# Optimization experiments

Measured on AMD Instinct MI355X. Metric: run time of the kernel, lower is better.

## Reference

```python
import jax, jax.numpy as jnp
import numpy as np

N, E, B, T, C_IN, K, F_CHEB, F_T, TS = 2000, 32000, 8, 12, 32, 3, 64, 64, 1
EPS = 1e-5  # torch nn.LayerNorm default


def setup_inputs() -> dict:
    key = jax.random.key(0)
    ks = jax.random.split(key, 12)
    X = jax.random.normal(ks[0], (B, N, C_IN, T), dtype=jnp.float32)
    edge_index = jax.random.randint(ks[1], (2, E), 0, N)
    edge_weight = jax.random.uniform(ks[2], (E,), dtype=jnp.float32)
    # lambda_max of L = D - A (PyG get_laplacian, normalization=None):
    # deg over source rows; power iteration emulates scipy.eigs(which='LM').
    src, dst = edge_index[0], edge_index[1]
    deg = jax.ops.segment_sum(edge_weight, src, num_segments=N)
    rows = jnp.concatenate([src, jnp.arange(N)])
    cols = jnp.concatenate([dst, jnp.arange(N)])
    wL = jnp.concatenate([-edge_weight, deg])
    v = jnp.ones((N,), jnp.float32) / np.sqrt(N)
    lam = jnp.float32(1.0)
    for _ in range(60):
        v2 = jax.ops.segment_sum(wL * v[cols], rows, num_segments=N)
        lam = jnp.linalg.norm(v2)
        v = v2 / (lam + 1e-12)
    lambda_max = lam.reshape(1)
    W_cheb = jax.random.normal(ks[3], (K, C_IN, F_CHEB), dtype=jnp.float32) * 0.1
    b_cheb = jax.random.uniform(ks[4], (F_CHEB,), dtype=jnp.float32) * 0.1
    time_w = jax.random.normal(ks[5], (F_T, F_CHEB, 1, 3), dtype=jnp.float32) * 0.05
    time_b = jax.random.uniform(ks[6], (F_T,), dtype=jnp.float32) * 0.1
    res_w = jax.random.normal(ks[7], (F_T, C_IN, 1, 1), dtype=jnp.float32) * 0.1
    res_b = jax.random.uniform(ks[8], (F_T,), dtype=jnp.float32) * 0.1
    ln_g = jnp.ones((F_T,), jnp.float32)
    ln_b = jnp.zeros((F_T,), jnp.float32)
    return dict(X=X, edge_index=edge_index, edge_weight=edge_weight,
                lambda_max=lambda_max, W_cheb=W_cheb, b_cheb=b_cheb,
                time_w=time_w, time_b=time_b, res_w=res_w, res_b=res_b,
                ln_g=ln_g, ln_b=ln_b)


def reference(X, edge_index, edge_weight, lambda_max, W_cheb, b_cheb,
              time_w, time_b, res_w, res_b, ln_g, ln_b):
    Bd, Nd, Cd, Td = X.shape
    src, dst = edge_index[0], edge_index[1]
    # L = D - A  (deg over source rows, matching PyG get_laplacian)
    deg = jax.ops.segment_sum(edge_weight, src, num_segments=Nd)
    srcs = jnp.concatenate([src, jnp.arange(Nd)])
    dsts = jnp.concatenate([dst, jnp.arange(Nd)])
    w = jnp.concatenate([-edge_weight, deg])
    w = 2.0 * w / lambda_max[0]
    w = w - (srcs == dsts).astype(w.dtype)  # L_hat = 2L/lmax - I

    # faithful to torch_geometric_temporal's permute+reshape of X into [T*B, N, C]
    Xt = jnp.transpose(X, (2, 0, 1, 3)).reshape(Nd, Cd, Td * Bd)
    x0 = Xt.transpose(0, 2, 1)  # node-major [N, T*B, C]

    def prop(h):  # out[dst] += w_e * h[src]  (PyG source_to_target flow)
        return jax.ops.segment_sum(w[:, None, None] * h[srcs], dsts, num_segments=Nd)

    # Chebyshev recursion: T0=x, T1=Lx, Tk=2L T(k-1) - T(k-2)
    out = jnp.einsum('nbc,cf->nbf', x0, W_cheb[0])
    Tx_prev = x0
    Tx = prop(x0)
    out = out + jnp.einsum('nbc,cf->nbf', Tx, W_cheb[1])
    for k in range(2, W_cheb.shape[0]):
        Tx_new = 2.0 * prop(Tx) - Tx_prev
        out = out + jnp.einsum('nbc,cf->nbf', Tx_new, W_cheb[k])
        Tx_prev, Tx = Tx, Tx_new
    out = jax.nn.relu(out + b_cheb)  # [N, T*B, F_cheb]

    # back to [B, N, F_cheb, T]
    Xc = out.transpose(0, 2, 1).reshape(Nd, -1, Bd, Td).transpose(2, 0, 1, 3)
    # temporal conv (1x3, pad (0,1), stride (1,TS)) on [B, F_cheb, N, T]
    h = jax.lax.conv_general_dilated(
        Xc.transpose(0, 2, 1, 3), time_w, (1, TS), ((0, 0), (1, 1)),
        dimension_numbers=('NCHW', 'OIHW', 'NCHW')) + time_b[None, :, None, None]
    # residual 1x1 conv on raw input
    r = jax.lax.conv_general_dilated(
        X.transpose(0, 2, 1, 3), res_w, (1, TS), ((0, 0), (0, 0)),
        dimension_numbers=('NCHW', 'OIHW', 'NCHW')) + res_b[None, :, None, None]
    z = jax.nn.relu(r + h).transpose(0, 3, 2, 1)  # [B, T, N, F_t]
    mu = z.mean(-1, keepdims=True)
    var = ((z - mu) ** 2).mean(-1, keepdims=True)
    z = (z - mu) / jnp.sqrt(var + EPS) * ln_g + ln_b
    return z.transpose(0, 2, 3, 1)  # [B, N, F_t, T]
```

## Files before the change

### kernel.cpp

```cpp
#include <hip/hip_runtime.h>
#include <hip/hip_bf16.h>

#define NN 2000
#define EE 32000
#define TT 12
#define CIN 32
#define FCH 64
#define TB 96
#define NODE_F 3072
#define NODE_F4 768

#define OFF_X0    0
#define OFF_TX1   6144000
#define OFF_CHEB  12288000
#define OFF_DEG   24576000
#define OFF_SW    24578000
#define OFF_ROWP  24580000
#define OFF_CNT   24582048
#define OFF_FILL  24584048
#define OFF_CCOL  24586048
#define OFF_CW    24618048
#define OFF_TWT   24650048
#define OFF_RWT   24662336

__device__ __forceinline__ float comp4(const float4& v, int i) {
  return i == 0 ? v.x : (i == 1 ? v.y : (i == 2 ? v.z : v.w));
}

__device__ __forceinline__ float b2f(unsigned short u) {
  return __uint_as_float(((unsigned)u) << 16);
}

__device__ __forceinline__ unsigned short f2b(float x) {
  __hip_bfloat16 h = __float2bfloat16(x);
  return *(unsigned short*)&h;
}

__global__ __launch_bounds__(256) void k_prep(const float* __restrict__ tw,
    const float* __restrict__ rw, unsigned short* __restrict__ twt,
    unsigned short* __restrict__ rwt) {
  int i = blockIdx.x * 256 + threadIdx.x;
  if (i < 12288) {
    int ft = i / 192;
    int r = i - ft * 192;
    twt[r * 64 + ft] = f2b(tw[i]);
  }
  if (i < 2048) {
    int ft = i >> 5;
    int c = i & 31;
    rwt[c * 64 + ft] = f2b(rw[i]);
  }
}

__global__ __launch_bounds__(256) void k_deg_cnt(const int* __restrict__ src,
    const int* __restrict__ dst, const float* __restrict__ ew,
    float* __restrict__ deg, int* __restrict__ cnt) {
  int e = blockIdx.x * 256 + threadIdx.x;
  if (e < EE) {
    atomicAdd(&deg[src[e]], ew[e]);
    atomicAdd(&cnt[dst[e]], 1);
  }
}

__global__ __launch_bounds__(256) void k_scan(const float* __restrict__ deg,
    const float* __restrict__ lam, const int* __restrict__ cnt,
    float* __restrict__ sw, int* __restrict__ rowp) {
  int tid = threadIdx.x;
  float s = 2.0f / lam[0];
  for (int n = tid; n < NN; n += 256) sw[n] = deg[n] * s - 1.0f;
  __shared__ int part[256];
  int base = tid * 8;
  int local[8];
  int sum = 0;
  #pragma unroll
  for (int i = 0; i < 8; ++i) {
    int idx = base + i;
    int v = (idx < NN) ? cnt[idx] : 0;
    local[i] = sum;
    sum += v;
  }
  part[tid] = sum;
  __syncthreads();
  for (int off = 1; off < 256; off <<= 1) {
    int v = part[tid];
    int add = (tid >= off) ? part[tid - off] : 0;
    __syncthreads();
    part[tid] = v + add;
    __syncthreads();
  }
  int excl = part[tid] - sum;
  #pragma unroll
  for (int i = 0; i < 8; ++i) {
    int idx = base + i;
    if (idx < NN) rowp[idx] = excl + local[i];
  }
  if (tid == 255) rowp[NN] = part[255];
}

__global__ __launch_bounds__(256) void k_fill(const int* __restrict__ src,
    const int* __restrict__ dst, const float* __restrict__ ew,
    const float* __restrict__ lam, const int* __restrict__ rowp,
    int* __restrict__ fill, int* __restrict__ ccol, float* __restrict__ cw) {
  int e = blockIdx.x * 256 + threadIdx.x;
  if (e < EE) {
    float s = 2.0f / lam[0];
    int d = dst[e], sn = src[e];
    int pos = rowp[d] + atomicAdd(&fill[d], 1);
    ccol[pos] = sn;
    cw[pos] = -ew[e] * s - ((sn == d) ? 1.0f : 0.0f);
  }
}

__global__ __launch_bounds__(256) void k_build_x0(const float* __restrict__ X,
                                                  float* __restrict__ x0) {
  int o = blockIdx.x * 256 + threadIdx.x;
  if (o >= NN * NODE_F) return;
  int n = o / NODE_F;
  int rem = o - n * NODE_F;
  int q = rem >> 5;
  int c2 = rem & 31;
  int g = n * NODE_F + c2 * TB + q;
  int ci = g / 192000;
  int r1 = g - ci * 192000;
  int b = r1 / 24000;
  int r2 = r1 - b * 24000;
  int nn2 = r2 / 12;
  int t = r2 - nn2 * 12;
  x0[o] = X[((b * NN + nn2) * CIN + ci) * TT + t];
}

__global__ __launch_bounds__(256) void k_prop1(const float* __restrict__ x0,
    const float* __restrict__ sw, const int* __restrict__ rowp,
    const int* __restrict__ ccol, const float* __restrict__ cw,
    float* __restrict__ tx1) {
  int n = blockIdx.x, tid = threadIdx.x;
  float s = sw[n];
  const float4* xb = (const float4*)x0;
  int own = n * NODE_F4 + tid * 3;
  float4 v0 = xb[own], v1 = xb[own + 1], v2 = xb[own + 2];
  float a[12];
  a[0]=s*v0.x; a[1]=s*v0.y; a[2]=s*v0.z; a[3]=s*v0.w;
  a[4]=s*v1.x; a[5]=s*v1.y; a[6]=s*v1.z; a[7]=s*v1.w;
  a[8]=s*v2.x; a[9]=s*v2.y; a[10]=s*v2.z; a[11]=s*v2.w;
  int rs = rowp[n], re = rowp[n + 1];
  for (int e = rs; e < re; ++e) {
    int c = ccol[e];
    float w = cw[e];
    int cb = c * NODE_F4 + tid * 3;
    float4 u0 = xb[cb], u1 = xb[cb + 1], u2 = xb[cb + 2];
    a[0]+=w*u0.x; a[1]+=w*u0.y; a[2]+=w*u0.z; a[3]+=w*u0.w;
    a[4]+=w*u1.x; a[5]+=w*u1.y; a[6]+=w*u1.z; a[7]+=w*u1.w;
    a[8]+=w*u2.x; a[9]+=w*u2.y; a[10]+=w*u2.z; a[11]+=w*u2.w;
  }
  float4* ob = (float4*)tx1;
  float4 o0, o1, o2;
  o0.x=a[0]; o0.y=a[1]; o0.z=a[2]; o0.w=a[3];
  o1.x=a[4]; o1.y=a[5]; o1.z=a[6]; o1.w=a[7];
  o2.x=a[8]; o2.y=a[9]; o2.z=a[10]; o2.w=a[11];
  ob[own] = o0; ob[own + 1] = o1; ob[own + 2] = o2;
}

__global__ __launch_bounds__(256) void k_cheb(const float* __restrict__ x0,
    const float* __restrict__ tx1, const float* __restrict__ sw,
    const int* __restrict__ rowp, const int* __restrict__ ccol,
    const float* __restrict__ cw, const float* __restrict__ Wc,
    const float* __restrict__ bc, float* __restrict__ cheb) {
  __shared__ float x0l[NODE_F];
  __shared__ float t1l[NODE_F];
  __shared__ float t2l[NODE_F];
  __shared__ __align__(16) unsigned short wl[3 * 2048];
  __shared__ float bl[64];
  int n = blockIdx.x, tid = threadIdx.x;
  {
    const float4* xs = (const float4*)(x0 + (size_t)n * NODE_F);
    const float4* ts = (const float4*)(tx1 + (size_t)n * NODE_F);
    float4* xd = (float4*)x0l;
    float4* td = (float4*)t1l;
    for (int i = tid; i < NODE_F4; i += 256) { xd[i] = xs[i]; td[i] = ts[i]; }
    for (int i = tid; i < 6144; i += 256) wl[i] = f2b(Wc[i]);
    if (tid < 64) bl[tid] = bc[tid];
  }
  float s = sw[n];
  float a[12];
  {
    const float4* tg4 = (const float4*)tx1 + (size_t)n * NODE_F4 + tid * 3;
    float4 v0 = tg4[0], v1 = tg4[1], v2 = tg4[2];
    a[0]=s*v0.x; a[1]=s*v0.y; a[2]=s*v0.z; a[3]=s*v0.w;
    a[4]=s*v1.x; a[5]=s*v1.y; a[6]=s*v1.z; a[7]=s*v1.w;
    a[8]=s*v2.x; a[9]=s*v2.y; a[10]=s*v2.z; a[11]=s*v2.w;
  }
  int rs = rowp[n], re = rowp[n + 1];
  const float4* xb = (const float4*)tx1;
  for (int e = rs; e < re; ++e) {
    int c = ccol[e];
    float w = cw[e];
    int cb = c * NODE_F4 + tid * 3;
    float4 u0 = xb[cb], u1 = xb[cb + 1], u2 = xb[cb + 2];
    a[0]+=w*u0.x; a[1]+=w*u0.y; a[2]+=w*u0.z; a[3]+=w*u0.w;
    a[4]+=w*u1.x; a[5]+=w*u1.y; a[6]+=w*u1.z; a[7]+=w*u1.w;
    a[8]+=w*u2.x; a[9]+=w*u2.y; a[10]+=w*u2.z; a[11]+=w*u2.w;
  }
  __syncthreads();
  #pragma unroll
  for (int j = 0; j < 12; ++j) t2l[tid * 12 + j] = 2.0f * a[j] - x0l[tid * 12 + j];
  __syncthreads();
  int f = tid & 63, qg = tid >> 6;
  float o[24];
  #pragma unroll
  for (int qi = 0; qi < 24; ++qi) o[qi] = bl[f];
  for (int cc = 0; cc < 4; ++cc) {
    float w0r[8], w1r[8], w2r[8];
    #pragma unroll
    for (int i = 0; i < 8; ++i) {
      int c = cc * 8 + i;
      w0r[i] = b2f(wl[c * 64 + f]);
      w1r[i] = b2f(wl[2048 + c * 64 + f]);
      w2r[i] = b2f(wl[4096 + c * 64 + f]);
    }
    #pragma unroll
    for (int qi = 0; qi < 24; ++qi) {
      int q = qi * 4 + qg;
      const float* xr = &x0l[q * 32 + cc * 8];
      const float* t1r = &t1l[q * 32 + cc * 8];
      const float* t2r = &t2l[q * 32 + cc * 8];
      float4 xv0 = *(const float4*)(xr);
      float4 xv1 = *(const float4*)(xr + 4);
      float4 y0 = *(const float4*)(t1r);
      float4 y1 = *(const float4*)(t1r + 4);
      float4 z0 = *(const float4*)(t2r);
      float4 z1 = *(const float4*)(t2r + 4);
      float acc = o[qi];
      #pragma unroll
      for (int i = 0; i < 4; ++i) {
        acc += comp4(xv0, i) * w0r[i] + comp4(y0, i) * w1r[i] + comp4(z0, i) * w2r[i];
        acc += comp4(xv1, i) * w0r[i + 4] + comp4(y1, i) * w1r[i + 4] + comp4(z1, i) * w2r[i + 4];
      }
      o[qi] = acc;
    }
  }
  float* cp = cheb + (size_t)n * TB * FCH;
  #pragma unroll
  for (int qi = 0; qi < 24; ++qi) {
    int q = qi * 4 + qg;
    cp[q * 64 + f] = fmaxf(o[qi], 0.0f);
  }
}

__global__ __launch_bounds__(256, 4) void k_final3(const float* __restrict__ X,
    const float* __restrict__ cheb, const unsigned short* __restrict__ twt,
    const unsigned short* __restrict__ rwt, const float* __restrict__ tb,
    const float* __restrict__ rb, const float* __restrict__ lg,
    const float* __restrict__ lb, float* __restrict__ out) {
  __shared__ float hp[4 * 12 * 64];
  __shared__ float zb[64 * 13];
  int tid = threadIdx.x;
  int f = tid & 63;
  int ntu = __builtin_amdgcn_readfirstlane(tid >> 6);

  float w0[16], w1[16], w2[16];
  #pragma unroll
  for (int i = 0; i < 16; ++i) {
    int fc = ntu * 16 + i;
    w0[i] = b2f(twt[(fc * 3 + 0) * 64 + f]);
    w1[i] = b2f(twt[(fc * 3 + 1) * 64 + f]);
    w2[i] = b2f(twt[(fc * 3 + 2) * 64 + f]);
  }
  float rwv[8];
  #pragma unroll
  for (int i = 0; i < 8; ++i) rwv[i] = b2f(rwt[(ntu * 8 + i) * 64 + f]);
  float tbf = tb[f], rbf = rb[f], lgf = lg[f], lbf = lb[f];
  float hbase = (ntu == 0) ? (tbf + rbf) : 0.0f;

  for (int it = 0; it < 16; ++it) {
    int p = blockIdx.x * 16 + it;
    int b = p / 2000;
    int n = p - b * 2000;
    float h[12];
    #pragma unroll
    for (int t = 0; t < 12; ++t) h[t] = hbase;
    {
      const float4* ch4 = (const float4*)(cheb + (size_t)n * 6144 + b * 768 + ntu * 16);
      #pragma unroll
      for (int r = 0; r < 12; ++r) {
        float4 sa = ch4[r * 16 + 0];
        float4 sb = ch4[r * 16 + 1];
        float4 sc = ch4[r * 16 + 2];
        float4 sd = ch4[r * 16 + 3];
        #pragma unroll
        for (int i = 0; i < 16; ++i) {
          float v = (i < 4) ? comp4(sa, i) : (i < 8) ? comp4(sb, i - 4)
                  : (i < 12) ? comp4(sc, i - 8) : comp4(sd, i - 12);
          if (r <= 10) h[r + 1] += w0[i] * v;
          h[r] += w1[i] * v;
          if (r >= 1) h[r - 1] += w2[i] * v;
        }
      }
    }
    {
      const float4* xp4 = (const float4*)(X + (size_t)p * 384 + ntu * 96);
      #pragma unroll
      for (int ci = 0; ci < 24; ++ci) {
        float4 xv = xp4[ci];
        #pragma unroll
        for (int k = 0; k < 4; ++k) {
          int idx = ci * 4 + k;
          h[idx % 12] += rwv[idx / 12] * comp4(xv, k);
        }
      }
    }
    #pragma unroll
    for (int t = 0; t < 12; ++t) hp[ntu * 768 + t * 64 + f] = h[t];
    __syncthreads();
    #pragma unroll
    for (int tt = 0; tt < 3; ++tt) {
      int t = ntu * 3 + tt;
      float v = hp[t * 64 + f] + hp[768 + t * 64 + f]
              + hp[1536 + t * 64 + f] + hp[2304 + t * 64 + f];
      v = fmaxf(v, 0.0f);
      float sum = v, sq = v * v;
      #pragma unroll
      for (int off = 32; off; off >>= 1) {
        sum += __shfl_xor(sum, off);
        sq += __shfl_xor(sq, off);
      }
      float mu = sum * (1.0f / 64.0f);
      float var = sq * (1.0f / 64.0f) - mu * mu;
      float inv = rsqrtf(var + 1e-5f);
      zb[f * 13 + t] = (v - mu) * inv * lgf + lbf;
    }
    __syncthreads();
    float* op = out + (size_t)p * 768;
    #pragma unroll
    for (int k = 0; k < 3; ++k) {
      int i = tid + k * 256;
      op[i] = zb[(i / 12) * 13 + i % 12];
    }
  }
}

extern "C" void kernel_launch(void* const* d_in, const int* in_sizes, int n_in,
                              void* d_out, int out_size, void* d_ws, size_t ws_size,
                              hipStream_t stream) {
  const float* X   = (const float*)d_in[0];
  const int*   ei  = (const int*)d_in[1];
  const float* ew  = (const float*)d_in[2];
  const float* lam = (const float*)d_in[3];
  const float* Wc  = (const float*)d_in[4];
  const float* bc  = (const float*)d_in[5];
  const float* tw  = (const float*)d_in[6];
  const float* tb  = (const float*)d_in[7];
  const float* rw  = (const float*)d_in[8];
  const float* rb  = (const float*)d_in[9];
  const float* lg  = (const float*)d_in[10];
  const float* lb  = (const float*)d_in[11];
  float* out = (float*)d_out;
  float* ws = (float*)d_ws;
  float* x0   = ws + OFF_X0;
  float* tx1  = ws + OFF_TX1;
  float* cheb = ws + OFF_CHEB;
  float* deg  = ws + OFF_DEG;
  float* swv  = ws + OFF_SW;
  int* rowp = (int*)(ws + OFF_ROWP);
  int* cnt  = (int*)(ws + OFF_CNT);
  int* fill = (int*)(ws + OFF_FILL);
  int* ccol = (int*)(ws + OFF_CCOL);
  float* cwv = ws + OFF_CW;
  unsigned short* twt = (unsigned short*)(ws + OFF_TWT);
  unsigned short* rwt = (unsigned short*)(ws + OFF_RWT);
  const int* srcp = ei;
  const int* dstp = ei + EE;

  hipMemsetAsync(deg, 0, (size_t)(OFF_CCOL - OFF_DEG) * sizeof(float), stream);
  k_prep<<<48, 256, 0, stream>>>(tw, rw, twt, rwt);
  k_deg_cnt<<<(EE + 255) / 256, 256, 0, stream>>>(srcp, dstp, ew, deg, cnt);
  k_scan<<<1, 256, 0, stream>>>(deg, lam, cnt, swv, rowp);
  k_fill<<<(EE + 255) / 256, 256, 0, stream>>>(srcp, dstp, ew, lam, rowp, fill, ccol, cwv);
  k_build_x0<<<(NN * NODE_F + 255) / 256, 256, 0, stream>>>(X, x0);
  k_prop1<<<NN, 256, 0, stream>>>(x0, swv, rowp, ccol, cwv, tx1);
  k_cheb<<<NN, 256, 0, stream>>>(x0, tx1, swv, rowp, ccol, cwv, Wc, bc, cheb);
  k_final3<<<1000, 256, 0, stream>>>(X, cheb, twt, rwt, tb, rb, lg, lb, out);
}
```

Baseline: 407.0 us.

## Store Chebyshev intermediates in bf16 and rebuild x0 transpose through LDS

The x0, Tx1 and Tx2 node feature buffers are now stored as packed bf16 pairs instead of fp32. This halves the bytes moved by the gather-heavy propagation kernels and by the LDS reads in the Chebyshev matmul. k_build_x0 now runs one block per node, loads contiguous float4s and transposes them through shared memory before writing packed bf16, replacing the old scattered per-element gather. k_final3 processes 8 node-batch pairs per block over 2000 blocks instead of 16 over 1000, and the lower precision on intermediates may add numerical error.

```diff
diff --git a/kernel.cpp b/kernel.cpp
--- a/kernel.cpp
+++ b/kernel.cpp
@@ -8,32 +8,35 @@
 #define FCH 64
 #define TB 96
 #define NODE_F 3072
-#define NODE_F4 768
-
-#define OFF_X0    0
-#define OFF_TX1   6144000
-#define OFF_CHEB  12288000
-#define OFF_DEG   24576000
-#define OFF_SW    24578000
-#define OFF_ROWP  24580000
-#define OFF_CNT   24582048
-#define OFF_FILL  24584048
-#define OFF_CCOL  24586048
-#define OFF_CW    24618048
-#define OFF_TWT   24650048
-#define OFF_RWT   24662336
+#define NODE_U 1536
+
+#define OFF_X0B   0
+#define OFF_TX1B  3072000
+#define OFF_CHEB  6144000
+#define OFF_DEG   18432000
+#define OFF_SW    18434000
+#define OFF_ROWP  18436000
+#define OFF_CNT   18438048
+#define OFF_FILL  18440048
+#define OFF_CCOL  18442048
+#define OFF_CW    18474048
+#define OFF_TWT   18506048
+#define OFF_RWT   18512192
 
 __device__ __forceinline__ float comp4(const float4& v, int i) {
   return i == 0 ? v.x : (i == 1 ? v.y : (i == 2 ? v.z : v.w));
 }
-
 __device__ __forceinline__ float b2f(unsigned short u) {
   return __uint_as_float(((unsigned)u) << 16);
 }
-
 __device__ __forceinline__ unsigned short f2b(float x) {
   __hip_bfloat16 h = __float2bfloat16(x);
   return *(unsigned short*)&h;
+}
+__device__ __forceinline__ float lo2f(unsigned u) { return __uint_as_float(u << 16); }
+__device__ __forceinline__ float hi2f(unsigned u) { return __uint_as_float(u & 0xffff0000u); }
+__device__ __forceinline__ unsigned pack2(float a, float b) {
+  return (unsigned)f2b(a) | ((unsigned)f2b(b) << 16);
 }
 
 __global__ __launch_bounds__(256) void k_prep(const float* __restrict__ tw,
@@ -112,97 +115,110 @@
 }
 
 __global__ __launch_bounds__(256) void k_build_x0(const float* __restrict__ X,
-                                                  float* __restrict__ x0) {
-  int o = blockIdx.x * 256 + threadIdx.x;
-  if (o >= NN * NODE_F) return;
-  int n = o / NODE_F;
-  int rem = o - n * NODE_F;
-  int q = rem >> 5;
-  int c2 = rem & 31;
-  int g = n * NODE_F + c2 * TB + q;
-  int ci = g / 192000;
-  int r1 = g - ci * 192000;
+                                                  unsigned* __restrict__ x0b) {
+  __shared__ float lds[32 * 97 + 32];
+  int n = blockIdx.x, r = threadIdx.x;
+  int G = n * NODE_F + r * 12;
+  int ci = G / 192000;
+  int r1 = G - ci * 192000;
   int b = r1 / 24000;
-  int r2 = r1 - b * 24000;
-  int nn2 = r2 / 12;
-  int t = r2 - nn2 * 12;
-  x0[o] = X[((b * NN + nn2) * CIN + ci) * TT + t];
-}
-
-__global__ __launch_bounds__(256) void k_prop1(const float* __restrict__ x0,
+  int nn2 = (r1 - b * 24000) / 12;
+  const float4* sp = (const float4*)(X + (((size_t)(b * NN + nn2) * CIN + ci) * TT));
+  float4 v0 = sp[0], v1 = sp[1], v2 = sp[2];
+  int c2 = r >> 3;
+  int qb = (r & 7) * 12;
+  float* d = &lds[c2 * 97 + qb];
+  d[0]=v0.x; d[1]=v0.y; d[2]=v0.z; d[3]=v0.w;
+  d[4]=v1.x; d[5]=v1.y; d[6]=v1.z; d[7]=v1.w;
+  d[8]=v2.x; d[9]=v2.y; d[10]=v2.z; d[11]=v2.w;
+  __syncthreads();
+  unsigned* op = x0b + (size_t)n * NODE_U;
+  #pragma unroll
+  for (int k = 0; k < 6; ++k) {
+    int i2 = r + k * 256;
+    int o0 = 2 * i2, o1 = 2 * i2 + 1;
+    float a0 = lds[(o0 & 31) * 97 + (o0 >> 5)];
+    float a1 = lds[(o1 & 31) * 97 + (o1 >> 5)];
+    op[i2] = pack2(a0, a1);
+  }
+}
+
+__global__ __launch_bounds__(256) void k_prop1(const unsigned* __restrict__ x0b,
     const float* __restrict__ sw, const int* __restrict__ rowp,
     const int* __restrict__ ccol, const float* __restrict__ cw,
-    float* __restrict__ tx1) {
+    unsigned* __restrict__ tx1b) {
   int n = blockIdx.x, tid = threadIdx.x;
   float s = sw[n];
-  const float4* xb = (const float4*)x0;
-  int own = n * NODE_F4 + tid * 3;
-  float4 v0 = xb[own], v1 = xb[own + 1], v2 = xb[own + 2];
   float a[12];
-  a[0]=s*v0.x; a[1]=s*v0.y; a[2]=s*v0.z; a[3]=s*v0.w;
-  a[4]=s*v1.x; a[5]=s*v1.y; a[6]=s*v1.z; a[7]=s*v1.w;
-  a[8]=s*v2.x; a[9]=s*v2.y; a[10]=s*v2.z; a[11]=s*v2.w;
+  {
+    const uint2* p = (const uint2*)(x0b + (size_t)n * NODE_U + tid * 6);
+    uint2 u0 = p[0], u1 = p[1], u2 = p[2];
+    a[0]=s*lo2f(u0.x); a[1]=s*hi2f(u0.x); a[2]=s*lo2f(u0.y); a[3]=s*hi2f(u0.y);
+    a[4]=s*lo2f(u1.x); a[5]=s*hi2f(u1.x); a[6]=s*lo2f(u1.y); a[7]=s*hi2f(u1.y);
+    a[8]=s*lo2f(u2.x); a[9]=s*hi2f(u2.x); a[10]=s*lo2f(u2.y); a[11]=s*hi2f(u2.y);
+  }
   int rs = rowp[n], re = rowp[n + 1];
   for (int e = rs; e < re; ++e) {
     int c = ccol[e];
     float w = cw[e];
-    int cb = c * NODE_F4 + tid * 3;
-    float4 u0 = xb[cb], u1 = xb[cb + 1], u2 = xb[cb + 2];
-    a[0]+=w*u0.x; a[1]+=w*u0.y; a[2]+=w*u0.z; a[3]+=w*u0.w;
-    a[4]+=w*u1.x; a[5]+=w*u1.y; a[6]+=w*u1.z; a[7]+=w*u1.w;
-    a[8]+=w*u2.x; a[9]+=w*u2.y; a[10]+=w*u2.z; a[11]+=w*u2.w;
-  }
-  float4* ob = (float4*)tx1;
-  float4 o0, o1, o2;
-  o0.x=a[0]; o0.y=a[1]; o0.z=a[2]; o0.w=a[3];
-  o1.x=a[4]; o1.y=a[5]; o1.z=a[6]; o1.w=a[7];
-  o2.x=a[8]; o2.y=a[9]; o2.z=a[10]; o2.w=a[11];
-  ob[own] = o0; ob[own + 1] = o1; ob[own + 2] = o2;
-}
-
-__global__ __launch_bounds__(256) void k_cheb(const float* __restrict__ x0,
-    const float* __restrict__ tx1, const float* __restrict__ sw,
+    const uint2* p = (const uint2*)(x0b + (size_t)c * NODE_U + tid * 6);
+    uint2 u0 = p[0], u1 = p[1], u2 = p[2];
+    a[0]+=w*lo2f(u0.x); a[1]+=w*hi2f(u0.x); a[2]+=w*lo2f(u0.y); a[3]+=w*hi2f(u0.y);
+    a[4]+=w*lo2f(u1.x); a[5]+=w*hi2f(u1.x); a[6]+=w*lo2f(u1.y); a[7]+=w*hi2f(u1.y);
+    a[8]+=w*lo2f(u2.x); a[9]+=w*hi2f(u2.x); a[10]+=w*lo2f(u2.y); a[11]+=w*hi2f(u2.y);
+  }
+  uint2* ob = (uint2*)(tx1b + (size_t)n * NODE_U + tid * 6);
+  ob[0] = make_uint2(pack2(a[0], a[1]), pack2(a[2], a[3]));
+  ob[1] = make_uint2(pack2(a[4], a[5]), pack2(a[6], a[7]));
+  ob[2] = make_uint2(pack2(a[8], a[9]), pack2(a[10], a[11]));
+}
+
+__global__ __launch_bounds__(256) void k_cheb(const unsigned* __restrict__ x0b,
+    const unsigned* __restrict__ tx1b, const float* __restrict__ sw,
     const int* __restrict__ rowp, const int* __restrict__ ccol,
     const float* __restrict__ cw, const float* __restrict__ Wc,
     const float* __restrict__ bc, float* __restrict__ cheb) {
-  __shared__ float x0l[NODE_F];
-  __shared__ float t1l[NODE_F];
-  __shared__ float t2l[NODE_F];
+  __shared__ __align__(16) unsigned x0l[NODE_U];
+  __shared__ __align__(16) unsigned t1l[NODE_U];
+  __shared__ __align__(16) unsigned t2l[NODE_U];
   __shared__ __align__(16) unsigned short wl[3 * 2048];
   __shared__ float bl[64];
   int n = blockIdx.x, tid = threadIdx.x;
   {
-    const float4* xs = (const float4*)(x0 + (size_t)n * NODE_F);
-    const float4* ts = (const float4*)(tx1 + (size_t)n * NODE_F);
-    float4* xd = (float4*)x0l;
-    float4* td = (float4*)t1l;
-    for (int i = tid; i < NODE_F4; i += 256) { xd[i] = xs[i]; td[i] = ts[i]; }
+    const uint4* xs = (const uint4*)(x0b + (size_t)n * NODE_U);
+    const uint4* ts = (const uint4*)(tx1b + (size_t)n * NODE_U);
+    uint4* xd = (uint4*)x0l;
+    uint4* td = (uint4*)t1l;
+    for (int i = tid; i < NODE_U / 4; i += 256) { xd[i] = xs[i]; td[i] = ts[i]; }
     for (int i = tid; i < 6144; i += 256) wl[i] = f2b(Wc[i]);
     if (tid < 64) bl[tid] = bc[tid];
   }
   float s = sw[n];
   float a[12];
   {
-    const float4* tg4 = (const float4*)tx1 + (size_t)n * NODE_F4 + tid * 3;
-    float4 v0 = tg4[0], v1 = tg4[1], v2 = tg4[2];
-    a[0]=s*v0.x; a[1]=s*v0.y; a[2]=s*v0.z; a[3]=s*v0.w;
-    a[4]=s*v1.x; a[5]=s*v1.y; a[6]=s*v1.z; a[7]=s*v1.w;
-    a[8]=s*v2.x; a[9]=s*v2.y; a[10]=s*v2.z; a[11]=s*v2.w;
+    const uint2* p = (const uint2*)(tx1b + (size_t)n * NODE_U + tid * 6);
+    uint2 u0 = p[0], u1 = p[1], u2 = p[2];
+    a[0]=s*lo2f(u0.x); a[1]=s*hi2f(u0.x); a[2]=s*lo2f(u0.y); a[3]=s*hi2f(u0.y);
+    a[4]=s*lo2f(u1.x); a[5]=s*hi2f(u1.x); a[6]=s*lo2f(u1.y); a[7]=s*hi2f(u1.y);
+    a[8]=s*lo2f(u2.x); a[9]=s*hi2f(u2.x); a[10]=s*lo2f(u2.y); a[11]=s*hi2f(u2.y);
   }
   int rs = rowp[n], re = rowp[n + 1];
-  const float4* xb = (const float4*)tx1;
   for (int e = rs; e < re; ++e) {
     int c = ccol[e];
     float w = cw[e];
-    int cb = c * NODE_F4 + tid * 3;
-    float4 u0 = xb[cb], u1 = xb[cb + 1], u2 = xb[cb + 2];
-    a[0]+=w*u0.x; a[1]+=w*u0.y; a[2]+=w*u0.z; a[3]+=w*u0.w;
-    a[4]+=w*u1.x; a[5]+=w*u1.y; a[6]+=w*u1.z; a[7]+=w*u1.w;
-    a[8]+=w*u2.x; a[9]+=w*u2.y; a[10]+=w*u2.z; a[11]+=w*u2.w;
+    const uint2* p = (const uint2*)(tx1b + (size_t)c * NODE_U + tid * 6);
+    uint2 u0 = p[0], u1 = p[1], u2 = p[2];
+    a[0]+=w*lo2f(u0.x); a[1]+=w*hi2f(u0.x); a[2]+=w*lo2f(u0.y); a[3]+=w*hi2f(u0.y);
+    a[4]+=w*lo2f(u1.x); a[5]+=w*hi2f(u1.x); a[6]+=w*lo2f(u1.y); a[7]+=w*hi2f(u1.y);
+    a[8]+=w*lo2f(u2.x); a[9]+=w*hi2f(u2.x); a[10]+=w*lo2f(u2.y); a[11]+=w*hi2f(u2.y);
   }
   __syncthreads();
   #pragma unroll
-  for (int j = 0; j < 12; ++j) t2l[tid * 12 + j] = 2.0f * a[j] - x0l[tid * 12 + j];
+  for (int k = 0; k < 6; ++k) {
+    unsigned ux = x0l[tid * 6 + k];
+    t2l[tid * 6 + k] = pack2(2.0f * a[2 * k] - lo2f(ux),
+                             2.0f * a[2 * k + 1] - hi2f(ux));
+  }
   __syncthreads();
   int f = tid & 63, qg = tid >> 6;
   float o[24];
@@ -220,21 +236,16 @@
     #pragma unroll
     for (int qi = 0; qi < 24; ++qi) {
       int q = qi * 4 + qg;
-      const float* xr = &x0l[q * 32 + cc * 8];
-      const float* t1r = &t1l[q * 32 + cc * 8];
-      const float* t2r = &t2l[q * 32 + cc * 8];
-      float4 xv0 = *(const float4*)(xr);
-      float4 xv1 = *(const float4*)(xr + 4);
-      float4 y0 = *(const float4*)(t1r);
-      float4 y1 = *(const float4*)(t1r + 4);
-      float4 z0 = *(const float4*)(t2r);
-      float4 z1 = *(const float4*)(t2r + 4);
+      uint4 ux = *(const uint4*)(&x0l[q * 16 + cc * 4]);
+      uint4 uy = *(const uint4*)(&t1l[q * 16 + cc * 4]);
+      uint4 uz = *(const uint4*)(&t2l[q * 16 + cc * 4]);
       float acc = o[qi];
-      #pragma unroll
-      for (int i = 0; i < 4; ++i) {
-        acc += comp4(xv0, i) * w0r[i] + comp4(y0, i) * w1r[i] + comp4(z0, i) * w2r[i];
-        acc += comp4(xv1, i) * w0r[i + 4] + comp4(y1, i) * w1r[i + 4] + comp4(z1, i) * w2r[i + 4];
-      }
+      acc += lo2f(ux.x)*w0r[0] + hi2f(ux.x)*w0r[1] + lo2f(ux.y)*w0r[2] + hi2f(ux.y)*w0r[3]
+           + lo2f(ux.z)*w0r[4] + hi2f(ux.z)*w0r[5] + lo2f(ux.w)*w0r[6] + hi2f(ux.w)*w0r[7];
+      acc += lo2f(uy.x)*w1r[0] + hi2f(uy.x)*w1r[1] + lo2f(uy.y)*w1r[2] + hi2f(uy.y)*w1r[3]
+           + lo2f(uy.z)*w1r[4] + hi2f(uy.z)*w1r[5] + lo2f(uy.w)*w1r[6] + hi2f(uy.w)*w1r[7];
+      acc += lo2f(uz.x)*w2r[0] + hi2f(uz.x)*w2r[1] + lo2f(uz.y)*w2r[2] + hi2f(uz.y)*w2r[3]
+           + lo2f(uz.z)*w2r[4] + hi2f(uz.z)*w2r[5] + lo2f(uz.w)*w2r[6] + hi2f(uz.w)*w2r[7];
       o[qi] = acc;
     }
   }
@@ -271,8 +282,8 @@
   float tbf = tb[f], rbf = rb[f], lgf = lg[f], lbf = lb[f];
   float hbase = (ntu == 0) ? (tbf + rbf) : 0.0f;
 
-  for (int it = 0; it < 16; ++it) {
-    int p = blockIdx.x * 16 + it;
+  for (int it = 0; it < 8; ++it) {
+    int p = blockIdx.x * 8 + it;
     int b = p / 2000;
     int n = p - b * 2000;
     float h[12];
@@ -355,8 +366,8 @@
   const float* lb  = (const float*)d_in[11];
   float* out = (float*)d_out;
   float* ws = (float*)d_ws;
-  float* x0   = ws + OFF_X0;
-  float* tx1  = ws + OFF_TX1;
+  unsigned* x0b  = (unsigned*)(ws + OFF_X0B);
+  unsigned* tx1b = (unsigned*)(ws + OFF_TX1B);
   float* cheb = ws + OFF_CHEB;
   float* deg  = ws + OFF_DEG;
   float* swv  = ws + OFF_SW;
@@ -375,8 +386,8 @@
   k_deg_cnt<<<(EE + 255) / 256, 256, 0, stream>>>(srcp, dstp, ew, deg, cnt);
   k_scan<<<1, 256, 0, stream>>>(deg, lam, cnt, swv, rowp);
   k_fill<<<(EE + 255) / 256, 256, 0, stream>>>(srcp, dstp, ew, lam, rowp, fill, ccol, cwv);
-  k_build_x0<<<(NN * NODE_F + 255) / 256, 256, 0, stream>>>(X, x0);
-  k_prop1<<<NN, 256, 0, stream>>>(x0, swv, rowp, ccol, cwv, tx1);
-  k_cheb<<<NN, 256, 0, stream>>>(x0, tx1, swv, rowp, ccol, cwv, Wc, bc, cheb);
-  k_final3<<<1000, 256, 0, stream>>>(X, cheb, twt, rwt, tb, rb, lg, lb, out);
-}
+  k_build_x0<<<NN, 256, 0, stream>>>(X, x0b);
+  k_prop1<<<NN, 256, 0, stream>>>(x0b, swv, rowp, ccol, cwv, tx1b);
+  k_cheb<<<NN, 256, 0, stream>>>(x0b, tx1b, swv, rowp, ccol, cwv, Wc, bc, cheb);
+  k_final3<<<2000, 256, 0, stream>>>(X, cheb, twt, rwt, tb, rb, lg, lb, out);
+}
```

Measured after the change: 510.0 us. +25.3%, slower.
